# Kernel tuning notes

Hardware: AMD Instinct MI355X
Metric: run time of the kernel (lower is better)

The kernel has to match this reference:

```python
import jax, jax.numpy as jnp
import numpy as np

B, S, HID = 2, 2048, 2048
NH, NKV, D = 32, 8, 64
G = NH // NKV
THETA = 150000.0


def rotate_half(x):
    x1, x2 = x[..., : D // 2], x[..., D // 2 :]
    return jnp.concatenate([-x2, x1], axis=-1)


def setup_inputs() -> dict:
    key = jax.random.key(0)
    ks = jax.random.split(key, 10)
    sc = 0.02
    return {
        "hidden_states": jax.random.normal(ks[0], (B, S, HID), jnp.float32),
        "position_ids": jnp.arange(S, dtype=jnp.int64 if jax.config.jax_enable_x64 else jnp.int32),
        "wq": jax.random.normal(ks[1], (HID, NH * D), jnp.float32) * sc,
        "bq": jax.random.normal(ks[2], (NH * D,), jnp.float32) * sc,
        "wk": jax.random.normal(ks[3], (HID, NKV * D), jnp.float32) * sc,
        "bk": jax.random.normal(ks[4], (NKV * D,), jnp.float32) * sc,
        "wv": jax.random.normal(ks[5], (HID, NKV * D), jnp.float32) * sc,
        "bv": jax.random.normal(ks[6], (NKV * D,), jnp.float32) * sc,
        "wo": jax.random.normal(ks[7], (NH * D, HID), jnp.float32) * sc,
        "bo": jax.random.normal(ks[8], (HID,), jnp.float32) * sc,
    }


def reference(hidden_states, position_ids, wq, bq, wk, bk, wv, bv, wo, bo):
    # projections: [B,S,NH,D] / [B,S,NKV,D] -> head-major
    q = (hidden_states @ wq + bq).reshape(B, S, NH, D).transpose(0, 2, 1, 3)   # [B,NH,S,D]
    k = (hidden_states @ wk + bk).reshape(B, S, NKV, D).transpose(0, 2, 1, 3)  # [B,NKV,S,D]
    v = (hidden_states @ wv + bv).reshape(B, S, NKV, D).transpose(0, 2, 1, 3)

    # HF RoPE: inv_freq over even dims, freqs duplicated across the two halves
    inv_freq = 1.0 / (THETA ** (jnp.arange(0, D, 2, dtype=jnp.float32) / D))   # [D/2]
    freqs = position_ids.astype(jnp.float32)[:, None] * inv_freq[None, :]      # [S,D/2]
    emb = jnp.concatenate([freqs, freqs], axis=-1)                             # [S,D]
    cos = jnp.cos(emb)[None, None]  # [1,1,S,D]
    sin = jnp.sin(emb)[None, None]
    q = q * cos + rotate_half(q) * sin
    k = k * cos + rotate_half(k) * sin

    # GQA: group query heads by kv head instead of repeat_interleave on K/V
    qg = q.reshape(B, NKV, G, S, D)
    scores = jnp.einsum("bkgsd,bktd->bkgst", qg, k) / jnp.sqrt(jnp.float32(D))  # [B,NKV,G,S,S]
    attn = jax.nn.softmax(scores, axis=-1)
    out = jnp.einsum("bkgst,bktd->bkgsd", attn, v)                              # [B,NKV,G,S,D]
    out = out.reshape(B, NH, S, D).transpose(0, 2, 1, 3).reshape(B, S, NH * D)  # [B,S,NH*D]
    return out @ wo + bo
```

## Files before the change

kernel.cpp:

```cpp
#include <hip/hip_runtime.h>
#include <hip/hip_bf16.h>
#include <math.h>

#define B_   2
#define S_   2048
#define HID_ 2048
#define NH_  32
#define NKV_ 8
#define D_   64
#define G_   (NH_/NKV_)
#define M_   (B_*S_)

typedef __hip_bfloat16 bf16;
typedef short bf16x8 __attribute__((ext_vector_type(8)));
typedef float f32x4  __attribute__((ext_vector_type(4)));
typedef unsigned short u16x4 __attribute__((ext_vector_type(4)));

__device__ inline unsigned short f2bfu(float f){
    __hip_bfloat16 h = __float2bfloat16(f);
    return __builtin_bit_cast(unsigned short, h);
}

__device__ __forceinline__ float fexp2(float x){
#if __has_builtin(__builtin_amdgcn_exp2f)
    return __builtin_amdgcn_exp2f(x);
#else
    return exp2f(x);
#endif
}

__device__ __forceinline__ void async16(const void* g, void* l) {
    __builtin_amdgcn_global_load_lds(
        (const __attribute__((address_space(1))) unsigned int*)g,
        (__attribute__((address_space(3))) unsigned int*)l, 16, 0, 0);
}

#define SWZ(r, c) ((c) ^ (((r) & 7) << 3))

#define S_BARRIER() asm volatile("s_barrier" ::: "memory")
__device__ __forceinline__ void vmwait4(){ asm volatile("s_waitcnt vmcnt(4)" ::: "memory"); }
__device__ __forceinline__ void vmwait0(){ asm volatile("s_waitcnt vmcnt(0)" ::: "memory"); }

__device__ __forceinline__ void wtrans_body(
    const float* __restrict__ s0, int N0,
    const float* __restrict__ s1, int N1,
    const float* __restrict__ s2, int N2,
    bf16* __restrict__ dst, int K, int bx, int by,
    unsigned short* __restrict__ tbuf)
{
    unsigned short (*t)[65] = (unsigned short (*)[65])tbuf;
    const int ntile = bx * 64, ktile = by * 64;
    const float* src; int nloc, Nseg;
    if (ntile < N0)           { src = s0; nloc = ntile;           Nseg = N0; }
    else if (ntile < N0 + N1) { src = s1; nloc = ntile - N0;      Nseg = N1; }
    else                      { src = s2; nloc = ntile - N0 - N1; Nseg = N2; }
    const int r  = threadIdx.x >> 4;
    const int c4 = (threadIdx.x & 15) * 4;
    #pragma unroll
    for (int p = 0; p < 4; p++) {
        const int k = p * 16 + r;
        const float4 f = *(const float4*)(src + (size_t)(ktile + k) * Nseg + nloc + c4);
        t[k][c4+0] = f2bfu(f.x); t[k][c4+1] = f2bfu(f.y);
        t[k][c4+2] = f2bfu(f.z); t[k][c4+3] = f2bfu(f.w);
    }
    __syncthreads();
    #pragma unroll
    for (int p = 0; p < 4; p++) {
        const int n = p * 16 + r;
        u16x4 u = { t[c4+0][n], t[c4+1][n], t[c4+2][n], t[c4+3][n] };
        *(u16x4*)((unsigned short*)dst + (size_t)(ntile + n) * K + ktile + c4) = u;
    }
}

__global__ __launch_bounds__(256) void prep_k(
    const float* __restrict__ hs, bf16* __restrict__ hs_b,
    const float* __restrict__ wq, const float* __restrict__ wk,
    const float* __restrict__ wv, bf16* __restrict__ wqkvT,
    const int* __restrict__ pos, float* __restrict__ ctab,
    float* __restrict__ stab)
{
    __shared__ unsigned short tbuf[64 * 65];
    const int bid = blockIdx.x;
    if (bid < 4096) {
        const int i = (bid * 256 + threadIdx.x) * 8;
        const float4 a = *(const float4*)(hs + i);
        const float4 b = *(const float4*)(hs + i + 4);
        uint4 u;
        u.x = (unsigned)f2bfu(a.x) | ((unsigned)f2bfu(a.y) << 16);
        u.y = (unsigned)f2bfu(a.z) | ((unsigned)f2bfu(a.w) << 16);
        u.z = (unsigned)f2bfu(b.x) | ((unsigned)f2bfu(b.y) << 16);
        u.w = (unsigned)f2bfu(b.z) | ((unsigned)f2bfu(b.w) << 16);
        *(uint4*)((unsigned short*)hs_b + i) = u;
    } else if (bid < 5632) {
        const int t = bid - 4096;
        wtrans_body(wq, 2048, wk, 512, wv, 512, wqkvT, HID_,
                    t % 48, t / 48, tbuf);
    } else {
        const int idx = (bid - 5632) * 256 + threadIdx.x;
        const int s = idx >> 5, i = idx & 31;
        const int is64 = (pos[1] == 0);
        const int p = is64 ? pos[2 * s] : pos[s];
        const double inv = exp(-(double)i * (log(150000.0) / 32.0));
        const double f = (double)p * inv;
        ctab[idx] = (float)cos(f);
        stab[idx] = (float)sin(f);
    }
}

__device__ __forceinline__ void slab64(
    const bf16* __restrict__ g, int grow0, int k0,
    unsigned short* lds, int wave, int lane)
{
    const int rr = wave * 8 + (lane >> 3);
    const int cc = ((lane & 7) ^ (lane >> 3)) * 8;
    async16(g + (size_t)(grow0 + rr) * 2048 + k0 + cc, lds + wave * 512);
}

template<int MODE, int BM>
__global__ __launch_bounds__(512, 2) void gemm4p_k(
    const bf16* __restrict__ A, const bf16* __restrict__ WT,
    const float* __restrict__ b0, const float* __restrict__ b1,
    const float* __restrict__ b2,
    bf16* __restrict__ Cq, bf16* __restrict__ Ck, bf16* __restrict__ Cv,
    float* __restrict__ Cout,
    const float* __restrict__ ctab, const float* __restrict__ stab)
{
    constexpr int MT = BM / 32;
    constexpr int PM = MT / 2;
    constexpr int LA = BM * 64;
    constexpr int LB = 256 * 64;
    constexpr int NT = 32;
    __shared__ unsigned short sA[2 * LA];
    __shared__ unsigned short sB[2 * LB];

    const int tid  = threadIdx.x;
    const int wave = tid >> 6, lane = tid & 63;
    const int li   = lane & 15, lj = lane >> 4;
    const int wm   = wave >> 2, wn = wave & 3;

    const int nbx = gridDim.x, nby = gridDim.y;
    const int lin = blockIdx.y * nbx + blockIdx.x;
    const int qq  = (nbx * nby) >> 3;
    const int logical = (lin & 7) * qq + (lin >> 3);
    const int m0 = (logical % nby) * BM;
    const int n0 = (logical / nby) * 256;
    const int swz = li & 7;

    f32x4 acc[MT][4];
    #pragma unroll
    for (int i = 0; i < MT; ++i)
        #pragma unroll
        for (int j = 0; j < 4; ++j)
            acc[i][j] = (f32x4){0.f, 0.f, 0.f, 0.f};

    bf16x8 bfr[4][2];

    auto stageAf = [&](int t) {
        unsigned short* l = sA + (t & 1) * LA;
        const int k0 = (t & (NT - 1)) * 64;
        #pragma unroll
        for (int i = 0; i < BM / 64; ++i)
            slab64(A, m0 + i * 64, k0, l + i * 64 * 64, wave, lane);
    };
    auto stageBf = [&](int t) {
        unsigned short* l = sB + (t & 1) * LB;
        const int k0 = (t & (NT - 1)) * 64;
        #pragma unroll
        for (int j = 0; j < 4; ++j)
            slab64(WT, n0 + j * 64, k0, l + j * 64 * 64, wave, lane);
    };
    auto ldB = [&](int tb_) {
        const unsigned short* base = sB + tb_ * LB;
        #pragma unroll
        for (int nt = 0; nt < 4; ++nt)
            #pragma unroll
            for (int ks = 0; ks < 2; ++ks)
                bfr[nt][ks] = *(const bf16x8*)
                    &base[(wn * 64 + nt * 16 + li) * 64 + ((ks * 4 + lj) ^ swz) * 8];
    };
    auto ldA = [&](int tb_, int h, bf16x8 (*af)[2]) {
        const unsigned short* base = sA + tb_ * LA;
        #pragma unroll
        for (int m = 0; m < PM; ++m)
            #pragma unroll
            for (int ks = 0; ks < 2; ++ks)
                af[m][ks] = *(const bf16x8*)
                    &base[(wm * (BM / 2) + (h * PM + m) * 16 + li) * 64
                          + ((ks * 4 + lj) ^ swz) * 8];
    };
    auto mfma_h = [&](int h, bf16x8 (*af)[2]) {
        __builtin_amdgcn_s_setprio(1);
        #pragma unroll
        for (int ks = 0; ks < 2; ++ks)
            #pragma unroll
            for (int m = 0; m < PM; ++m)
                #pragma unroll
                for (int nt = 0; nt < 4; ++nt)
                    acc[h * PM + m][nt] = __builtin_amdgcn_mfma_f32_16x16x32_bf16(
                        af[m][ks], bfr[nt][ks], acc[h * PM + m][nt], 0, 0, 0);
        __builtin_amdgcn_s_setprio(0);
    };

    stageAf(0); stageBf(0); stageBf(1);
    vmwait4();
    S_BARRIER();

    for (int i = 0; i < NT / 2; ++i) {
        const int ta = 2 * i, tb = 2 * i + 1;
        bf16x8 afh[PM][2];
        ldB(0); ldA(0, 0, afh);
        stageAf(tb);
        S_BARRIER(); mfma_h(0, afh); S_BARRIER();
        ldA(0, 1, afh);
        stageBf(ta + 2);
        S_BARRIER(); mfma_h(1, afh);
        vmwait4();
        S_BARRIER();
        ldB(1); ldA(1, 0, afh);
        stageAf(ta + 2);
        S_BARRIER(); mfma_h(0, afh); S_BARRIER();
        ldA(1, 1, afh);
        stageBf(tb + 2);
        S_BARRIER(); mfma_h(1, afh);
        vmwait4();
        S_BARRIER();
    }
    vmwait0();
    S_BARRIER();

    if (MODE == 1) {
        #pragma unroll
        for (int mt = 0; mt < MT; ++mt)
            #pragma unroll
            for (int nt = 0; nt < 4; ++nt) {
                const int col = n0 + wn * 64 + nt * 16 + li;
                const float bb = b0[col];
                #pragma unroll
                for (int r = 0; r < 4; ++r) {
                    const int row = m0 + wm * (BM / 2) + mt * 16 + lj * 4 + r;
                    Cout[(size_t)row * HID_ + col] = acc[mt][nt][r] + bb;
                }
            }
        return;
    }

    int seg, cb; const float* bias;
    if (n0 < 2048)      { seg = 0; cb = n0;        bias = b0; }
    else if (n0 < 2560) { seg = 1; cb = n0 - 2048; bias = b1; }
    else                { seg = 2; cb = n0 - 2560; bias = b2; }

    float bl[4];
    #pragma unroll
    for (int nt = 0; nt < 4; ++nt) bl[nt] = bias[cb + wn * 64 + nt * 16 + li];

    if (seg == 2) {
        const int b = m0 >> 11;
        #pragma unroll
        for (int nt = 0; nt < 4; ++nt) {
            const int cseg = cb + wn * 64 + nt * 16 + li;
            const int hv = cseg >> 6, d = cseg & 63;
            #pragma unroll
            for (int mt = 0; mt < MT; ++mt) {
                const int sb = (m0 & (S_ - 1)) + wm * (BM / 2) + mt * 16 + lj * 4;
                u16x4 u = { f2bfu(acc[mt][nt][0] + bl[nt]),
                            f2bfu(acc[mt][nt][1] + bl[nt]),
                            f2bfu(acc[mt][nt][2] + bl[nt]),
                            f2bfu(acc[mt][nt][3] + bl[nt]) };
                *(u16x4*)((unsigned short*)Cv +
                    ((size_t)((b * NKV_ + hv) * 64 + d)) * S_ + sb) = u;
            }
        }
        return;
    }

    const float qs = (seg == 0) ? 0.18033688011112042f : 1.0f;
    #pragma unroll
    for (int mt = 0; mt < MT; ++mt) {
        #pragma unroll
        for (int r = 0; r < 4; ++r) {
            const int row = m0 + wm * (BM / 2) + mt * 16 + lj * 4 + r;
            const int s = row & (S_ - 1);
            const float c0  = ctab[s * 32 + li],      sn0 = stab[s * 32 + li];
            const float c1  = ctab[s * 32 + 16 + li], sn1 = stab[s * 32 + 16 + li];
            const float x0 = acc[mt][0][r] + bl[0];
            const float x1 = acc[mt][1][r] + bl[1];
            const float x2 = acc[mt][2][r] + bl[2];
            const float x3 = acc[mt][3][r] + bl[3];
            const float y0 = (x0 * c0 - x2 * sn0) * qs;
            const float y2 = (x2 * c0 + x0 * sn0) * qs;
            const float y1 = (x1 * c1 - x3 * sn1) * qs;
            const float y3 = (x3 * c1 + x1 * sn1) * qs;
            if (seg == 0) {
                bf16* cp = Cq + (size_t)row * HID_ + n0 + wn * 64 + li;
                cp[0]  = __float2bfloat16(y0);
                cp[16] = __float2bfloat16(y1);
                cp[32] = __float2bfloat16(y2);
                cp[48] = __float2bfloat16(y3);
            } else {
                bf16* cp = Ck + (size_t)row * 512 + cb + wn * 64 + li;
                cp[0]  = __float2bfloat16(y0);
                cp[16] = __float2bfloat16(y1);
                cp[32] = __float2bfloat16(y2);
                cp[48] = __float2bfloat16(y3);
            }
        }
    }
}

__global__ __launch_bounds__(256, 2) void attn_k(
    const bf16* __restrict__ qws, const bf16* __restrict__ kws,
    const bf16* __restrict__ vtw, bf16* __restrict__ ows,
    const float* __restrict__ wo, bf16* __restrict__ woT)
{
    __shared__ unsigned short sMem[24576];

    if (blockIdx.y >= 64) {
        const int t = (blockIdx.y - 64) * 8 + blockIdx.x;
        wtrans_body(wo, 2048, wo, 0, wo, 0, woT, HID_, t & 31, t >> 5, sMem);
        return;
    }

    unsigned short* sK  = sMem;
    unsigned short* sVt = sMem + 4096;
    unsigned short* sP  = sMem + 8192;

    const int tid  = threadIdx.x;
    const int wave = tid >> 6, lane = tid & 63;
    const int li   = lane & 15, lj = lane >> 4;
    const int bh   = blockIdx.y;
    const int q0   = blockIdx.x * 256;
    const int b    = bh / NH_, h = bh % NH_;
    const int hk   = h / G_;

    bf16x8 qf[4][2];
    #pragma unroll
    for (int g = 0; g < 4; g++) {
        const bf16* qp = qws + (size_t)(b * S_ + q0 + wave * 64 + g * 16 + li) * HID_
                         + h * D_ + lj * 8;
        qf[g][0] = *(const bf16x8*)(qp);
        qf[g][1] = *(const bf16x8*)(qp + 32);
    }

    f32x4 o[4][4];
    #pragma unroll
    for (int g = 0; g < 4; g++)
        #pragma unroll
        for (int mt = 0; mt < 4; mt++) o[g][mt] = (f32x4){0.f, 0.f, 0.f, 0.f};
    float mr[4] = {-1e30f, -1e30f, -1e30f, -1e30f};
    float ll[4] = {0.f, 0.f, 0.f, 0.f};

    const int srow = tid >> 2, scol = (tid & 3) * 16;
    const bf16* kb = kws + (size_t)b * S_ * 512 + hk * 64;
    const bf16* vb = vtw + (size_t)((b * NKV_ + hk) * 64) * S_;
    unsigned short* sp = sP + wave * (64 * 64);

    uint4 pk0, pk1, pv0, pv1;
    {
        const uint4* kp = (const uint4*)(kb + (size_t)srow * 512 + scol);
        const uint4* vp = (const uint4*)(vb + (size_t)srow * S_ + scol);
        pk0 = kp[0]; pk1 = kp[1]; pv0 = vp[0]; pv1 = vp[1];
    }

    for (int kt = 0; kt < S_; kt += 64) {
        __syncthreads();
        *(uint4*)&sK [srow * 64 + SWZ(srow, scol)]     = pk0;
        *(uint4*)&sK [srow * 64 + SWZ(srow, scol + 8)] = pk1;
        *(uint4*)&sVt[srow * 64 + SWZ(srow, scol)]     = pv0;
        *(uint4*)&sVt[srow * 64 + SWZ(srow, scol + 8)] = pv1;
        __syncthreads();

        if (kt + 64 < S_) {
            const uint4* kp = (const uint4*)(kb + (size_t)(kt + 64 + srow) * 512 + scol);
            const uint4* vp = (const uint4*)(vb + (size_t)srow * S_ + kt + 64 + scol);
            pk0 = kp[0]; pk1 = kp[1]; pv0 = vp[0]; pv1 = vp[1];
        }

        bf16x8 kf[4][2];
        #pragma unroll
        for (int nt = 0; nt < 4; nt++)
            #pragma unroll
            for (int ks = 0; ks < 2; ks++)
                kf[nt][ks] = *(const bf16x8*)&sK[(nt * 16 + li) * 64
                                                 + SWZ(li, ks * 32 + lj * 8)];

        f32x4 c[4][4];
        __builtin_amdgcn_s_setprio(1);
        #pragma unroll
        for (int g = 0; g < 4; g++)
            #pragma unroll
            for (int nt = 0; nt < 4; nt++) {
                f32x4 t = (f32x4){0.f, 0.f, 0.f, 0.f};
                t = __builtin_amdgcn_mfma_f32_16x16x32_bf16(kf[nt][0], qf[g][0], t, 0, 0, 0);
                t = __builtin_amdgcn_mfma_f32_16x16x32_bf16(kf[nt][1], qf[g][1], t, 0, 0, 0);
                c[g][nt] = t;
            }
        __builtin_amdgcn_s_setprio(0);

        bf16x8 vf[4][2];
        #pragma unroll
        for (int mt = 0; mt < 4; mt++)
            #pragma unroll
            for (int ks = 0; ks < 2; ks++)
                vf[mt][ks] = *(const bf16x8*)&sVt[(mt * 16 + li) * 64
                                                  + SWZ(li, ks * 32 + lj * 8)];

        #pragma unroll
        for (int g = 0; g < 4; g++) {
            float m0a = fmaxf(fmaxf(c[g][0][0], c[g][0][1]),
                              fmaxf(c[g][0][2], c[g][0][3]));
            float m1a = fmaxf(fmaxf(c[g][1][0], c[g][1][1]),
                              fmaxf(c[g][1][2], c[g][1][3]));
            float m2a = fmaxf(fmaxf(c[g][2][0], c[g][2][1]),
                              fmaxf(c[g][2][2], c[g][2][3]));
            float m3a = fmaxf(fmaxf(c[g][3][0], c[g][3][1]),
                              fmaxf(c[g][3][2], c[g][3][3]));
            float cm = fmaxf(fmaxf(m0a, m1a), fmaxf(m2a, m3a));
            cm = fmaxf(cm, __shfl_xor(cm, 16));
            cm = fmaxf(cm, __shfl_xor(cm, 32));
            if (!__all(cm - mr[g] <= 8.0f)) {
                const float mnew = fmaxf(mr[g], cm);
                const float al   = fexp2(mr[g] - mnew);
                mr[g] = mnew;
                ll[g] *= al;
                #pragma unroll
                for (int mt = 0; mt < 4; mt++) o[g][mt] *= al;
            }
            float rs = 0.f;
            #pragma unroll
            for (int nt = 0; nt < 4; nt++) {
                const float e0 = fexp2(c[g][nt][0] - mr[g]);
                const float e1 = fexp2(c[g][nt][1] - mr[g]);
                const float e2 = fexp2(c[g][nt][2] - mr[g]);
                const float e3 = fexp2(c[g][nt][3] - mr[g]);
                rs += (e0 + e1) + (e2 + e3);
                u16x4 u = { f2bfu(e0), f2bfu(e1), f2bfu(e2), f2bfu(e3) };
                *(u16x4*)&sp[(g * 16 + li) * 64 + SWZ(li, nt * 16 + lj * 4)] = u;
            }
            ll[g] += rs;
        }

        __builtin_amdgcn_s_setprio(1);
        #pragma unroll
        for (int g = 0; g < 4; g++) {
            #pragma unroll
            for (int ks = 0; ks < 2; ks++) {
                const bf16x8 pf = *(const bf16x8*)&sp[(g * 16 + li) * 64
                                                      + SWZ(li, ks * 32 + lj * 8)];
                #pragma unroll
                for (int mt = 0; mt < 4; mt++)
                    o[g][mt] = __builtin_amdgcn_mfma_f32_16x16x32_bf16(
                        vf[mt][ks], pf, o[g][mt], 0, 0, 0);
            }
        }
        __builtin_amdgcn_s_setprio(0);
    }

    #pragma unroll
    for (int g = 0; g < 4; g++) {
        float l = ll[g];
        l += __shfl_xor(l, 16);
        l += __shfl_xor(l, 32);
        const float inv = 1.0f / l;
        bf16* op = ows + (size_t)(b * S_ + q0 + wave * 64 + g * 16 + li) * HID_ + h * D_;
        #pragma unroll
        for (int mt = 0; mt < 4; mt++) {
            u16x4 u = { f2bfu(o[g][mt][0] * inv), f2bfu(o[g][mt][1] * inv),
                        f2bfu(o[g][mt][2] * inv), f2bfu(o[g][mt][3] * inv) };
            *(u16x4*)((unsigned short*)op + mt * 16 + lj * 4) = u;
        }
    }
}

extern "C" void kernel_launch(void* const* d_in, const int* in_sizes, int n_in,
                              void* d_out, int out_size, void* d_ws, size_t ws_size,
                              hipStream_t stream)
{
    const float* hs  = (const float*)d_in[0];
    const int*   pos = (const int*)d_in[1];
    const float* wq = (const float*)d_in[2];
    const float* bq = (const float*)d_in[3];
    const float* wk = (const float*)d_in[4];
    const float* bk = (const float*)d_in[5];
    const float* wv = (const float*)d_in[6];
    const float* bv = (const float*)d_in[7];
    const float* wo = (const float*)d_in[8];
    const float* bo = (const float*)d_in[9];

    char* ws = (char*)d_ws;
    float* ctab  = (float*)(ws);
    float* stab  = (float*)(ws + (256u << 10));
    bf16*  k_ws  = (bf16*)(ws + (512u << 10));
    bf16*  v_t   = (bf16*)(ws + (512u << 10) + (4u  << 20));
    bf16*  q_ws  = (bf16*)(ws + (512u << 10) + (8u  << 20));
    bf16*  hs_b  = (bf16*)(ws + (512u << 10) + (24u << 20));
    bf16*  o_ws  = hs_b;
    bf16*  wqkvT = (bf16*)(ws + (512u << 10) + (40u << 20));
    bf16*  woT   = wqkvT;

    prep_k<<<dim3(5888), dim3(256), 0, stream>>>(
        hs, hs_b, wq, wk, wv, wqkvT, pos, ctab, stab);

    gemm4p_k<0, 256><<<dim3(12, 16), dim3(512), 0, stream>>>(
        hs_b, wqkvT, bq, bk, bv, q_ws, k_ws, v_t, nullptr, ctab, stab);

    attn_k<<<dim3(8, 192), dim3(256), 0, stream>>>(
        q_ws, k_ws, v_t, o_ws, wo, woT);

    gemm4p_k<1, 128><<<dim3(8, 32), dim3(512), 0, stream>>>(
        o_ws, woT, bo, nullptr, nullptr, nullptr, nullptr, nullptr,
        (float*)d_out, nullptr, nullptr);
}
```

Baseline: 324.3 us.

## Double-buffer K/V tiles with async global-to-LDS loads in attention

Replaces register-staged K/V prefetch with direct asynchronous global-to-LDS copies into a double-buffered shared tile, waiting on vmcnt before a single barrier per iteration. It also interleaves the QK^T MFMAs with the softmax per query group and defers the V fragment loads, which lowers peak register pressure. The cost is more LDS (64KB per block), which may limit occupancy at two blocks per CU. The swizzle layout of async16 destinations must match the SWZ used when reading fragments.

```diff
diff --git a/kernel.cpp b/kernel.cpp
--- a/kernel.cpp
+++ b/kernel.cpp
@@ -312,7 +312,7 @@
     const bf16* __restrict__ vtw, bf16* __restrict__ ows,
     const float* __restrict__ wo, bf16* __restrict__ woT)
 {
-    __shared__ unsigned short sMem[24576];
+    __shared__ unsigned short sMem[32768];
 
     if (blockIdx.y >= 64) {
         const int t = (blockIdx.y - 64) * 8 + blockIdx.x;
@@ -320,9 +320,7 @@
         return;
     }
 
-    unsigned short* sK  = sMem;
-    unsigned short* sVt = sMem + 4096;
-    unsigned short* sP  = sMem + 8192;
+    unsigned short* sP = sMem + 16384;
 
     const int tid  = threadIdx.x;
     const int wave = tid >> 6, lane = tid & 63;
@@ -349,31 +347,37 @@
     float mr[4] = {-1e30f, -1e30f, -1e30f, -1e30f};
     float ll[4] = {0.f, 0.f, 0.f, 0.f};
 
-    const int srow = tid >> 2, scol = (tid & 3) * 16;
     const bf16* kb = kws + (size_t)b * S_ * 512 + hk * 64;
     const bf16* vb = vtw + (size_t)((b * NKV_ + hk) * 64) * S_;
     unsigned short* sp = sP + wave * (64 * 64);
 
-    uint4 pk0, pk1, pv0, pv1;
-    {
-        const uint4* kp = (const uint4*)(kb + (size_t)srow * 512 + scol);
-        const uint4* vp = (const uint4*)(vb + (size_t)srow * S_ + scol);
-        pk0 = kp[0]; pk1 = kp[1]; pv0 = vp[0]; pv1 = vp[1];
-    }
-
+    const int rr = wave * 8 + (lane >> 3);
+    const int cc = ((lane & 7) ^ (lane >> 3)) * 8;
+
+    auto stageKV = [&](int ktn, int buf) {
+        unsigned short* dK = sMem + buf * 8192;
+        unsigned short* dV = dK + 4096;
+        #pragma unroll
+        for (int rd = 0; rd < 2; rd++) {
+            const int r = rd * 32 + rr;
+            async16(kb + (size_t)(ktn + r) * 512 + cc, dK + rd * 2048 + wave * 512);
+            async16(vb + (size_t)r * S_ + ktn + cc,    dV + rd * 2048 + wave * 512);
+        }
+    };
+
+    stageKV(0, 0);
     for (int kt = 0; kt < S_; kt += 64) {
-        __syncthreads();
-        *(uint4*)&sK [srow * 64 + SWZ(srow, scol)]     = pk0;
-        *(uint4*)&sK [srow * 64 + SWZ(srow, scol + 8)] = pk1;
-        *(uint4*)&sVt[srow * 64 + SWZ(srow, scol)]     = pv0;
-        *(uint4*)&sVt[srow * 64 + SWZ(srow, scol + 8)] = pv1;
-        __syncthreads();
+        const int buf = (kt >> 6) & 1;
+        const unsigned short* sK  = sMem + buf * 8192;
+        const unsigned short* sVt = sK + 4096;
 
         if (kt + 64 < S_) {
-            const uint4* kp = (const uint4*)(kb + (size_t)(kt + 64 + srow) * 512 + scol);
-            const uint4* vp = (const uint4*)(vb + (size_t)srow * S_ + kt + 64 + scol);
-            pk0 = kp[0]; pk1 = kp[1]; pv0 = vp[0]; pv1 = vp[1];
-        }
+            stageKV(kt + 64, buf ^ 1);
+            vmwait4();
+        } else {
+            vmwait0();
+        }
+        S_BARRIER();
 
         bf16x8 kf[4][2];
         #pragma unroll
@@ -383,38 +387,25 @@
                 kf[nt][ks] = *(const bf16x8*)&sK[(nt * 16 + li) * 64
                                                  + SWZ(li, ks * 32 + lj * 8)];
 
-        f32x4 c[4][4];
-        __builtin_amdgcn_s_setprio(1);
-        #pragma unroll
-        for (int g = 0; g < 4; g++)
+        #pragma unroll
+        for (int g = 0; g < 4; g++) {
+            f32x4 c[4];
+            __builtin_amdgcn_s_setprio(1);
             #pragma unroll
             for (int nt = 0; nt < 4; nt++) {
-                f32x4 t = (f32x4){0.f, 0.f, 0.f, 0.f};
-                t = __builtin_amdgcn_mfma_f32_16x16x32_bf16(kf[nt][0], qf[g][0], t, 0, 0, 0);
-                t = __builtin_amdgcn_mfma_f32_16x16x32_bf16(kf[nt][1], qf[g][1], t, 0, 0, 0);
-                c[g][nt] = t;
-            }
-        __builtin_amdgcn_s_setprio(0);
-
-        bf16x8 vf[4][2];
-        #pragma unroll
-        for (int mt = 0; mt < 4; mt++)
-            #pragma unroll
-            for (int ks = 0; ks < 2; ks++)
-                vf[mt][ks] = *(const bf16x8*)&sVt[(mt * 16 + li) * 64
-                                                  + SWZ(li, ks * 32 + lj * 8)];
-
-        #pragma unroll
-        for (int g = 0; g < 4; g++) {
-            float m0a = fmaxf(fmaxf(c[g][0][0], c[g][0][1]),
-                              fmaxf(c[g][0][2], c[g][0][3]));
-            float m1a = fmaxf(fmaxf(c[g][1][0], c[g][1][1]),
-                              fmaxf(c[g][1][2], c[g][1][3]));
-            float m2a = fmaxf(fmaxf(c[g][2][0], c[g][2][1]),
-                              fmaxf(c[g][2][2], c[g][2][3]));
-            float m3a = fmaxf(fmaxf(c[g][3][0], c[g][3][1]),
-                              fmaxf(c[g][3][2], c[g][3][3]));
-            float cm = fmaxf(fmaxf(m0a, m1a), fmaxf(m2a, m3a));
+                c[nt] = (f32x4){0.f, 0.f, 0.f, 0.f};
+                #pragma unroll
+                for (int ks = 0; ks < 2; ks++)
+                    c[nt] = __builtin_amdgcn_mfma_f32_16x16x32_bf16(
+                        kf[nt][ks], qf[g][ks], c[nt], 0, 0, 0);
+            }
+            __builtin_amdgcn_s_setprio(0);
+
+            float cm = c[0][0];
+            #pragma unroll
+            for (int nt = 0; nt < 4; nt++)
+                #pragma unroll
+                for (int r = 0; r < 4; r++) cm = fmaxf(cm, c[nt][r]);
             cm = fmaxf(cm, __shfl_xor(cm, 16));
             cm = fmaxf(cm, __shfl_xor(cm, 32));
             if (!__all(cm - mr[g] <= 8.0f)) {
@@ -428,16 +419,24 @@
             float rs = 0.f;
             #pragma unroll
             for (int nt = 0; nt < 4; nt++) {
-                const float e0 = fexp2(c[g][nt][0] - mr[g]);
-                const float e1 = fexp2(c[g][nt][1] - mr[g]);
-                const float e2 = fexp2(c[g][nt][2] - mr[g]);
-                const float e3 = fexp2(c[g][nt][3] - mr[g]);
+                const float e0 = fexp2(c[nt][0] - mr[g]);
+                const float e1 = fexp2(c[nt][1] - mr[g]);
+                const float e2 = fexp2(c[nt][2] - mr[g]);
+                const float e3 = fexp2(c[nt][3] - mr[g]);
                 rs += (e0 + e1) + (e2 + e3);
                 u16x4 u = { f2bfu(e0), f2bfu(e1), f2bfu(e2), f2bfu(e3) };
                 *(u16x4*)&sp[(g * 16 + li) * 64 + SWZ(li, nt * 16 + lj * 4)] = u;
             }
             ll[g] += rs;
         }
+
+        bf16x8 vf[4][2];
+        #pragma unroll
+        for (int mt = 0; mt < 4; mt++)
+            #pragma unroll
+            for (int ks = 0; ks < 2; ks++)
+                vf[mt][ks] = *(const bf16x8*)&sVt[(mt * 16 + li) * 64
+                                                  + SWZ(li, ks * 32 + lj * 8)];
 
         __builtin_amdgcn_s_setprio(1);
         #pragma unroll
@@ -453,6 +452,8 @@
             }
         }
         __builtin_amdgcn_s_setprio(0);
+
+        S_BARRIER();
     }
 
     #pragma unroll
```

New measurement: 324.8 us. About the same (+0.1%).
